# Optimization experiments

Hardware: AMD Instinct MI355X
Metric: run time of the kernel (lower is better)

Reference implementation:

```python
import jax, jax.numpy as jnp
import numpy as np

N_TOKENS = 4096   # flattened batch*seq tokens
D_MODEL = 1024
N_EXPERT = 8
D_HIDDEN = 1024   # expert FFN hidden size
TOP_K = 2


def setup_inputs() -> dict:
    key = jax.random.key(0)
    ks = jax.random.split(key, 4)
    f32 = jnp.float32
    return {
        "inp": jax.random.normal(ks[0], (N_TOKENS, D_MODEL), f32),
        "gate_w": jax.random.normal(ks[1], (D_MODEL, N_EXPERT), f32) * 0.02,
        "gate_b": jnp.zeros((N_EXPERT,), f32),
        "w1": jax.random.normal(ks[2], (N_EXPERT, D_MODEL, D_HIDDEN), f32) * 0.02,
        "b1": jnp.zeros((N_EXPERT, D_HIDDEN), f32),
        "w2": jax.random.normal(ks[3], (N_EXPERT, D_HIDDEN, D_MODEL), f32) * 0.02,
        "b2": jnp.zeros((N_EXPERT, D_MODEL), f32),
    }


def reference(inp, gate_w, gate_b, w1, b1, w2, b2):
    """FMoE forward: NaiveGate top-k -> dispatch -> per-expert FFN -> weighted combine.

    Math is identical to dispatch/grouped-GEMM/gather: since both top-k slots of a
    token see the same input, out[n] = sum_e coeff[n,e] * expert_e(inp[n]) where
    coeff[n,e] = sum_k softmax(top_vals)[n,k] * 1[top_idx[n,k] == e].
    """
    n_expert = gate_w.shape[-1]
    # NaiveGate: linear gate, top-k, softmax over the k selected logits
    logits = inp @ gate_w + gate_b                      # [N, E]
    top_val, top_idx = jax.lax.top_k(logits, TOP_K)     # [N, K]
    score = jax.nn.softmax(top_val, axis=-1)            # [N, K]
    # combine weights per (token, expert); top-k indices are distinct per token
    coeff = jnp.sum(
        jax.nn.one_hot(top_idx, n_expert, dtype=inp.dtype) * score[..., None],
        axis=1,
    )                                                   # [N, E]
    # expert FFN (exact-erf GeLU, matching torch.nn.functional.gelu)
    h = jax.nn.gelu(jnp.einsum('nd,edh->neh', inp, w1) + b1, approximate=False)  # [N, E, H]
    out = jnp.einsum('neh,ehd->nd', h * coeff[:, :, None], w2) + coeff @ b2      # [N, D]
    return out


if __name__ == "__main__":
    out = reference(**setup_inputs())
    print(out.shape, out.dtype)
```

## Files before the change

kernel.cpp:

```cpp
#include <hip/hip_runtime.h>
#include <math.h>

#define N_TOKENS 4096
#define D_MODEL  1024
#define N_EXPERT 8
#define D_HIDDEN 1024
#define N_POS    8192

typedef __bf16 bf16x8 __attribute__((ext_vector_type(8)));
typedef float  f32x4  __attribute__((ext_vector_type(4)));
typedef unsigned short u16x8 __attribute__((ext_vector_type(8)));

#define GLOBAL_AS __attribute__((address_space(1)))
#define LDS_AS    __attribute__((address_space(3)))

static __device__ __forceinline__ void async_ld16(const void* g, void* l) {
    __builtin_amdgcn_global_load_lds((GLOBAL_AS void*)g, (LDS_AS void*)l, 16, 0, 0);
}

static __device__ __forceinline__ unsigned short f2bf(float f) {
    unsigned int u = __builtin_bit_cast(unsigned int, f);
    u += 0x7fffu + ((u >> 16) & 1u);
    return (unsigned short)(u >> 16);
}
static __device__ __forceinline__ unsigned int pack2(float a, float b) {
    return (unsigned int)f2bf(a) | ((unsigned int)f2bf(b) << 16);
}
static __device__ __forceinline__ float bflo(unsigned int u) {
    return __builtin_bit_cast(float, u << 16);
}
static __device__ __forceinline__ float bfhi(unsigned int u) {
    return __builtin_bit_cast(float, u & 0xffff0000u);
}

__global__ __launch_bounds__(256) void convert_transpose_kernel(
    const float* __restrict__ w1, const float* __restrict__ w2,
    unsigned short* __restrict__ w1b, unsigned short* __restrict__ w2b)
{
    int mat = blockIdx.z;
    const float* src = (mat < 8) ? (w1 + (size_t)mat * 1048576)
                                 : (w2 + (size_t)(mat - 8) * 1048576);
    unsigned short* dst = (mat < 8) ? (w1b + (size_t)mat * 1048576)
                                    : (w2b + (size_t)(mat - 8) * 1048576);
    __shared__ float tile[64][68];
    int r0 = blockIdx.x * 64, c0 = blockIdx.y * 64;
    int tid = threadIdx.x;
    #pragma unroll
    for (int i = 0; i < 4; ++i) {
        int r = (tid >> 4) + i * 16;
        float4 v = *(const float4*)(src + (size_t)(r0 + r) * 1024 + c0 + (tid & 15) * 4);
        *(float4*)&tile[r][(tid & 15) * 4] = v;
    }
    __syncthreads();
    int dr = tid >> 2;
    #pragma unroll
    for (int p = 0; p < 2; ++p) {
        int ch = (tid & 3) + p * 4;
        u16x8 o;
        #pragma unroll
        for (int j = 0; j < 8; ++j) o[j] = f2bf(tile[ch * 8 + j][dr]);
        *(u16x8*)(dst + (size_t)(c0 + dr) * 1024 + r0 + ch * 8) = o;
    }
}

__global__ __launch_bounds__(256) void gate_kernel(
    const float* __restrict__ inp, const float* __restrict__ gate_w,
    const float* __restrict__ gate_b, int* __restrict__ cnts,
    int* __restrict__ emeta, float* __restrict__ stok)
{
    __shared__ int bcnt[8], base[8];
    __shared__ int tinfo[16];
    int tid = threadIdx.x, lane = tid & 63, wave = tid >> 6;
    if (tid < 8) bcnt[tid] = 0;
    __syncthreads();

    for (int t = 0; t < 4; ++t) {
        int ti = wave * 4 + t;
        int n  = blockIdx.x * 16 + ti;
        const float* ip = inp + (size_t)n * D_MODEL;
        float acc[8] = {0.f,0.f,0.f,0.f,0.f,0.f,0.f,0.f};
        for (int d0 = lane * 4; d0 < D_MODEL; d0 += 256) {
            float4 x = *(const float4*)(ip + d0);
            #pragma unroll
            for (int j = 0; j < 4; ++j) {
                float xv = (j == 0) ? x.x : (j == 1) ? x.y : (j == 2) ? x.z : x.w;
                float4 g0 = *(const float4*)(gate_w + (d0 + j) * 8);
                float4 g1 = *(const float4*)(gate_w + (d0 + j) * 8 + 4);
                acc[0] += xv * g0.x; acc[1] += xv * g0.y;
                acc[2] += xv * g0.z; acc[3] += xv * g0.w;
                acc[4] += xv * g1.x; acc[5] += xv * g1.y;
                acc[6] += xv * g1.z; acc[7] += xv * g1.w;
            }
        }
        #pragma unroll
        for (int off = 32; off > 0; off >>= 1)
            #pragma unroll
            for (int e = 0; e < 8; ++e)
                acc[e] += __shfl_xor(acc[e], off, 64);
        #pragma unroll
        for (int e = 0; e < 8; ++e) acc[e] += gate_b[e];

        int e0 = 0; float v0 = acc[0];
        #pragma unroll
        for (int e = 1; e < 8; ++e) if (acc[e] > v0) { v0 = acc[e]; e0 = e; }
        int e1 = -1; float v1 = -1e30f;
        #pragma unroll
        for (int e = 0; e < 8; ++e) if (e != e0 && acc[e] > v1) { v1 = acc[e]; e1 = e; }
        float tv = expf(v1 - v0);
        float s0 = 1.0f / (1.0f + tv);
        float s1 = tv / (1.0f + tv);

        if (lane == 0) {
            int r0 = atomicAdd(&bcnt[e0], 1);
            int r1 = atomicAdd(&bcnt[e1], 1);
            tinfo[ti] = e0 | (e1 << 4) | (r0 << 8) | (r1 << 20);
            stok[2 * n]     = s0;
            stok[2 * n + 1] = s1;
        }
    }
    __syncthreads();
    if (tid < 8) base[tid] = atomicAdd(&cnts[tid], bcnt[tid]);
    __syncthreads();
    if (tid < 16) {
        int n = blockIdx.x * 16 + tid;
        unsigned int inf = (unsigned int)tinfo[tid];
        int e0 = inf & 15, e1 = (inf >> 4) & 15;
        int p0 = base[e0] + ((inf >> 8) & 4095);
        int p1 = base[e1] + (int)(inf >> 20);
        emeta[n] = e0 | (e1 << 4) | (p0 << 8) | (p1 << 20);
    }
}

__global__ __launch_bounds__(256) void gather_kernel(
    const float* __restrict__ inp, const int* __restrict__ cnts,
    const int* __restrict__ emeta, unsigned short* __restrict__ Ag,
    int* __restrict__ tok2pos)
{
    int lane = threadIdx.x & 63, wave = threadIdx.x >> 6;
    int n = blockIdx.x * 4 + wave;
    unsigned int em = (unsigned int)emeta[n];
    int e0 = em & 15, e1 = (em >> 4) & 15;
    int p0 = (em >> 8) & 4095, p1 = (int)(em >> 20);
    int off0 = 0, off1 = 0;
    #pragma unroll
    for (int e = 0; e < 8; ++e) {
        int c = cnts[e];
        off0 += (e < e0) ? c : 0;
        off1 += (e < e1) ? c : 0;
    }
    int pos0 = off0 + p0, pos1 = off1 + p1;
    if (lane == 0) {
        tok2pos[2 * n]     = pos0;
        tok2pos[2 * n + 1] = pos1;
    }
    const float* ip = inp + (size_t)n * D_MODEL;
    unsigned short* r0 = Ag + (size_t)pos0 * D_MODEL;
    unsigned short* r1 = Ag + (size_t)pos1 * D_MODEL;
    for (int d = lane * 4; d < D_MODEL; d += 256) {
        float4 v = *(const float4*)(ip + d);
        uint2 u; u.x = pack2(v.x, v.y); u.y = pack2(v.z, v.w);
        *(uint2*)(r0 + d) = u;
        *(uint2*)(r1 + d) = u;
    }
}

__global__ __launch_bounds__(256, 4) void ffn1_kernel(
    const unsigned short* __restrict__ Ag, const unsigned short* __restrict__ w1b,
    const float* __restrict__ b1, const int* __restrict__ cnts,
    unsigned short* __restrict__ Hg)
{
    int bid = blockIdx.x;
    int e = bid & 7, nt = (bid >> 3) & 15, mt = bid >> 7;
    int off = 0, Ne = 0;
    #pragma unroll
    for (int i = 0; i < 8; ++i) {
        int c = cnts[i];
        off += (i < e) ? c : 0;
        Ne = (i == e) ? c : Ne;
    }
    int m0 = mt * 128;
    if (m0 >= Ne) return;
    int n0 = nt * 64;

    __shared__ unsigned short As[2 * 128 * 32];
    __shared__ unsigned short Bs[2 * 64 * 32];

    int tid = threadIdx.x, lane = tid & 63, wave = tid >> 6;
    int lrow = lane >> 2, lchunk = lane & 3;
    int csw8 = (lchunk ^ ((lrow >> 1) & 3)) * 8;

    int ga0 = off + m0 + wave * 32 + lrow;
    int ga1 = ga0 + 16;
    if (ga0 >= N_POS) ga0 = N_POS - 1;
    if (ga1 >= N_POS) ga1 = N_POS - 1;
    const unsigned short* aS0 = Ag + (size_t)ga0 * D_MODEL + csw8;
    const unsigned short* aS1 = Ag + (size_t)ga1 * D_MODEL + csw8;
    const unsigned short* bS = w1b + (size_t)e * D_MODEL * D_HIDDEN
                             + (size_t)(n0 + wave * 16 + lrow) * D_MODEL + csw8;
    unsigned short* aD0 = &As[(wave * 32) * 32];
    unsigned short* aD1 = &As[(wave * 32 + 16) * 32];
    unsigned short* bD  = &Bs[(wave * 16) * 32];

    f32x4 acc[4][2] = {};
    int wm = (wave & 1) * 64, wn = ((wave >> 1) & 1) * 32;
    int lane15 = lane & 15, quad = lane >> 4;
    int fro = (quad ^ ((lane15 >> 1) & 3)) * 8;

    for (int k0 = 0; k0 < D_MODEL; k0 += 64) {
        #pragma unroll
        for (int h = 0; h < 2; ++h) {
            int ko = k0 + h * 32;
            async_ld16(aS0 + ko, aD0 + h * 4096);
            async_ld16(aS1 + ko, aD1 + h * 4096);
            async_ld16(bS  + ko, bD  + h * 2048);
        }
        __syncthreads();
        #pragma unroll
        for (int h = 0; h < 2; ++h) {
            bf16x8 af[4], bf[2];
            #pragma unroll
            for (int t = 0; t < 4; ++t)
                af[t] = *(const bf16x8*)&As[h * 4096 + (wm + t * 16 + lane15) * 32 + fro];
            #pragma unroll
            for (int t = 0; t < 2; ++t)
                bf[t] = *(const bf16x8*)&Bs[h * 2048 + (wn + t * 16 + lane15) * 32 + fro];
            #pragma unroll
            for (int i = 0; i < 4; ++i)
                #pragma unroll
                for (int j = 0; j < 2; ++j)
                    acc[i][j] = __builtin_amdgcn_mfma_f32_16x16x32_bf16(
                        af[i], bf[j], acc[i][j], 0, 0, 0);
        }
        __syncthreads();
    }

    const float* bexp = b1 + (size_t)e * D_HIDDEN;
    #pragma unroll
    for (int j = 0; j < 2; ++j) {
        int gcol = n0 + wn + j * 16 + lane15;
        float bv = bexp[gcol];
        #pragma unroll
        for (int i = 0; i < 4; ++i) {
            int rowb = wm + i * 16 + quad * 4;
            #pragma unroll
            for (int r = 0; r < 4; ++r) {
                int row = rowb + r;
                if (m0 + row < Ne) {
                    float x = acc[i][j][r] + bv;
                    float gv = 0.5f * x * (1.0f + erff(x * 0.70710678118654752f));
                    Hg[(size_t)(off + m0 + row) * D_HIDDEN + gcol] = f2bf(gv);
                }
            }
        }
    }
}

__global__ __launch_bounds__(256, 4) void ffn2_kernel(
    const unsigned short* __restrict__ Hg, const unsigned short* __restrict__ w2b,
    const int* __restrict__ cnts, unsigned short* __restrict__ Og)
{
    int bid = blockIdx.x;
    int e = bid & 7, nt = (bid >> 3) & 15, mt = bid >> 7;
    int off = 0, Ne = 0;
    #pragma unroll
    for (int i = 0; i < 8; ++i) {
        int c = cnts[i];
        off += (i < e) ? c : 0;
        Ne = (i == e) ? c : Ne;
    }
    int m0 = mt * 128;
    if (m0 >= Ne) return;
    int n0 = nt * 64;

    __shared__ unsigned short As[2 * 128 * 32];
    __shared__ unsigned short Bs[2 * 64 * 32];

    int tid = threadIdx.x, lane = tid & 63, wave = tid >> 6;
    int lrow = lane >> 2, lchunk = lane & 3;
    int csw8 = (lchunk ^ ((lrow >> 1) & 3)) * 8;

    int ga0 = off + m0 + wave * 32 + lrow;
    int ga1 = ga0 + 16;
    if (ga0 >= N_POS) ga0 = N_POS - 1;
    if (ga1 >= N_POS) ga1 = N_POS - 1;
    const unsigned short* aS0 = Hg + (size_t)ga0 * D_HIDDEN + csw8;
    const unsigned short* aS1 = Hg + (size_t)ga1 * D_HIDDEN + csw8;
    const unsigned short* bS = w2b + (size_t)e * D_HIDDEN * D_MODEL
                             + (size_t)(n0 + wave * 16 + lrow) * D_HIDDEN + csw8;
    unsigned short* aD0 = &As[(wave * 32) * 32];
    unsigned short* aD1 = &As[(wave * 32 + 16) * 32];
    unsigned short* bD  = &Bs[(wave * 16) * 32];

    f32x4 acc[4][2] = {};
    int wm = (wave & 1) * 64, wn = ((wave >> 1) & 1) * 32;
    int lane15 = lane & 15, quad = lane >> 4;
    int fro = (quad ^ ((lane15 >> 1) & 3)) * 8;

    for (int k0 = 0; k0 < D_HIDDEN; k0 += 64) {
        #pragma unroll
        for (int h = 0; h < 2; ++h) {
            int ko = k0 + h * 32;
            async_ld16(aS0 + ko, aD0 + h * 4096);
            async_ld16(aS1 + ko, aD1 + h * 4096);
            async_ld16(bS  + ko, bD  + h * 2048);
        }
        __syncthreads();
        #pragma unroll
        for (int h = 0; h < 2; ++h) {
            bf16x8 af[4], bf[2];
            #pragma unroll
            for (int t = 0; t < 4; ++t)
                af[t] = *(const bf16x8*)&As[h * 4096 + (wm + t * 16 + lane15) * 32 + fro];
            #pragma unroll
            for (int t = 0; t < 2; ++t)
                bf[t] = *(const bf16x8*)&Bs[h * 2048 + (wn + t * 16 + lane15) * 32 + fro];
            #pragma unroll
            for (int i = 0; i < 4; ++i)
                #pragma unroll
                for (int j = 0; j < 2; ++j)
                    acc[i][j] = __builtin_amdgcn_mfma_f32_16x16x32_bf16(
                        af[i], bf[j], acc[i][j], 0, 0, 0);
        }
        __syncthreads();
    }

    #pragma unroll
    for (int j = 0; j < 2; ++j) {
        int gcol = n0 + wn + j * 16 + lane15;
        #pragma unroll
        for (int i = 0; i < 4; ++i) {
            int rowb = wm + i * 16 + quad * 4;
            #pragma unroll
            for (int r = 0; r < 4; ++r) {
                int row = rowb + r;
                if (m0 + row < Ne) {
                    Og[(size_t)(off + m0 + row) * D_MODEL + gcol] =
                        f2bf(acc[i][j][r]);
                }
            }
        }
    }
}

__global__ __launch_bounds__(256) void combine_kernel(
    const unsigned short* __restrict__ Og, const int* __restrict__ tok2pos,
    const float* __restrict__ stok, const int* __restrict__ emeta,
    const float* __restrict__ b2, float* __restrict__ out)
{
    int lane = threadIdx.x & 63, wave = threadIdx.x >> 6;
    int n = blockIdx.x * 4 + wave;
    int pos0 = tok2pos[2 * n], pos1 = tok2pos[2 * n + 1];
    float s0 = stok[2 * n], s1 = stok[2 * n + 1];
    unsigned int em = (unsigned int)emeta[n];
    int e0 = em & 15, e1 = (em >> 4) & 15;
    const unsigned short* o0 = Og + (size_t)pos0 * D_MODEL;
    const unsigned short* o1 = Og + (size_t)pos1 * D_MODEL;
    const float* bA = b2 + (size_t)e0 * D_MODEL;
    const float* bB = b2 + (size_t)e1 * D_MODEL;
    float* op = out + (size_t)n * D_MODEL;
    for (int d = lane * 4; d < D_MODEL; d += 256) {
        uint2 u0 = *(const uint2*)(o0 + d);
        uint2 u1 = *(const uint2*)(o1 + d);
        float4 xa = *(const float4*)(bA + d);
        float4 xb = *(const float4*)(bB + d);
        float4 r;
        r.x = s0 * (bflo(u0.x) + xa.x) + s1 * (bflo(u1.x) + xb.x);
        r.y = s0 * (bfhi(u0.x) + xa.y) + s1 * (bfhi(u1.x) + xb.y);
        r.z = s0 * (bflo(u0.y) + xa.z) + s1 * (bflo(u1.y) + xb.z);
        r.w = s0 * (bfhi(u0.y) + xa.w) + s1 * (bfhi(u1.y) + xb.w);
        *(float4*)(op + d) = r;
    }
}

extern "C" void kernel_launch(void* const* d_in, const int* in_sizes, int n_in,
                              void* d_out, int out_size, void* d_ws, size_t ws_size,
                              hipStream_t stream) {
    const float* inp    = (const float*)d_in[0];
    const float* gate_w = (const float*)d_in[1];
    const float* gate_b = (const float*)d_in[2];
    const float* w1     = (const float*)d_in[3];
    const float* b1     = (const float*)d_in[4];
    const float* w2     = (const float*)d_in[5];
    const float* b2     = (const float*)d_in[6];
    float* out = (float*)d_out;

    char* ws = (char*)d_ws;
    int*   cnts    = (int*)  (ws);
    int*   emeta   = (int*)  (ws + 4096);
    float* stok    = (float*)(ws + 65536);
    int*   tok2pos = (int*)  (ws + 131072);
    unsigned short* w2b = (unsigned short*)(ws + 1048576);
    unsigned short* Hg  = (unsigned short*)(ws + 17825792);
    unsigned short* w1b = (unsigned short*)(ws + 34603008);
    unsigned short* Og  = (unsigned short*)(ws + 34603008);

    unsigned short* Ag = (unsigned short*)d_out;

    hipMemsetAsync(cnts, 0, N_EXPERT * sizeof(int), stream);
    convert_transpose_kernel<<<dim3(16, 16, 16), 256, 0, stream>>>(w1, w2, w1b, w2b);
    gate_kernel<<<dim3(N_TOKENS / 16), 256, 0, stream>>>(
        inp, gate_w, gate_b, cnts, emeta, stok);
    gather_kernel<<<dim3(N_TOKENS / 4), 256, 0, stream>>>(
        inp, cnts, emeta, Ag, tok2pos);
    ffn1_kernel<<<dim3(4096), 256, 0, stream>>>(Ag, w1b, b1, cnts, Hg);
    ffn2_kernel<<<dim3(4096), 256, 0, stream>>>(Hg, w2b, cnts, Og);
    combine_kernel<<<dim3(N_TOKENS / 4), 256, 0, stream>>>(
        Og, tok2pos, stok, emeta, b2, out);
}
```

Before: 224.9 us.

## Replace gather copy with indexed A-loads in ffn1 via pos2tok map

Instead of materializing a permuted bf16 copy of the input per expert slot, the input is converted to bf16 once in the weight-conversion kernel. A small plan kernel then writes a position-to-token map, and ffn1 loads A rows indirectly through that map. The cnts memset is folded into the conversion kernel, the trailing __syncthreads in both GEMM loops is skipped on the last iteration, and combine recomputes positions from counts instead of reading tok2pos. This removes one launch and the gather's duplicated 16MB bf16 write, at the cost of scattered row loads in ffn1.

```diff
diff --git a/kernel.cpp b/kernel.cpp
--- a/kernel.cpp
+++ b/kernel.cpp
@@ -33,18 +33,36 @@
     return __builtin_bit_cast(float, u & 0xffff0000u);
 }
 
-__global__ __launch_bounds__(256) void convert_transpose_kernel(
+__global__ __launch_bounds__(256) void convert_kernel(
     const float* __restrict__ w1, const float* __restrict__ w2,
-    unsigned short* __restrict__ w1b, unsigned short* __restrict__ w2b)
-{
+    const float* __restrict__ inp,
+    unsigned short* __restrict__ w1b, unsigned short* __restrict__ w2b,
+    unsigned short* __restrict__ inp_bf, int* __restrict__ cnts)
+{
+    int tid = threadIdx.x;
+    if (blockIdx.x == 0 && blockIdx.y == 0 && blockIdx.z == 0 && tid < 8)
+        cnts[tid] = 0;
     int mat = blockIdx.z;
+    int r0 = blockIdx.x * 64, c0 = blockIdx.y * 64;
+
+    if (mat >= 16) {
+        const float* src = inp + (size_t)(mat - 16) * 1048576;
+        unsigned short* dst = inp_bf + (size_t)(mat - 16) * 1048576;
+        #pragma unroll
+        for (int i = 0; i < 4; ++i) {
+            int r = (tid >> 4) + i * 16;
+            float4 v = *(const float4*)(src + (size_t)(r0 + r) * 1024 + c0 + (tid & 15) * 4);
+            uint2 u; u.x = pack2(v.x, v.y); u.y = pack2(v.z, v.w);
+            *(uint2*)(dst + (size_t)(r0 + r) * 1024 + c0 + (tid & 15) * 4) = u;
+        }
+        return;
+    }
+
     const float* src = (mat < 8) ? (w1 + (size_t)mat * 1048576)
                                  : (w2 + (size_t)(mat - 8) * 1048576);
     unsigned short* dst = (mat < 8) ? (w1b + (size_t)mat * 1048576)
                                     : (w2b + (size_t)(mat - 8) * 1048576);
     __shared__ float tile[64][68];
-    int r0 = blockIdx.x * 64, c0 = blockIdx.y * 64;
-    int tid = threadIdx.x;
     #pragma unroll
     for (int i = 0; i < 4; ++i) {
         int r = (tid >> 4) + i * 16;
@@ -131,13 +149,11 @@
     }
 }
 
-__global__ __launch_bounds__(256) void gather_kernel(
-    const float* __restrict__ inp, const int* __restrict__ cnts,
-    const int* __restrict__ emeta, unsigned short* __restrict__ Ag,
-    int* __restrict__ tok2pos)
-{
-    int lane = threadIdx.x & 63, wave = threadIdx.x >> 6;
-    int n = blockIdx.x * 4 + wave;
+__global__ __launch_bounds__(256) void plan_kernel(
+    const int* __restrict__ cnts, const int* __restrict__ emeta,
+    int* __restrict__ pos2tok)
+{
+    int n = blockIdx.x * 256 + threadIdx.x;
     unsigned int em = (unsigned int)emeta[n];
     int e0 = em & 15, e1 = (em >> 4) & 15;
     int p0 = (em >> 8) & 4095, p1 = (int)(em >> 20);
@@ -148,26 +164,14 @@
         off0 += (e < e0) ? c : 0;
         off1 += (e < e1) ? c : 0;
     }
-    int pos0 = off0 + p0, pos1 = off1 + p1;
-    if (lane == 0) {
-        tok2pos[2 * n]     = pos0;
-        tok2pos[2 * n + 1] = pos1;
-    }
-    const float* ip = inp + (size_t)n * D_MODEL;
-    unsigned short* r0 = Ag + (size_t)pos0 * D_MODEL;
-    unsigned short* r1 = Ag + (size_t)pos1 * D_MODEL;
-    for (int d = lane * 4; d < D_MODEL; d += 256) {
-        float4 v = *(const float4*)(ip + d);
-        uint2 u; u.x = pack2(v.x, v.y); u.y = pack2(v.z, v.w);
-        *(uint2*)(r0 + d) = u;
-        *(uint2*)(r1 + d) = u;
-    }
+    pos2tok[off0 + p0] = n;
+    pos2tok[off1 + p1] = n;
 }
 
 __global__ __launch_bounds__(256, 4) void ffn1_kernel(
-    const unsigned short* __restrict__ Ag, const unsigned short* __restrict__ w1b,
+    const unsigned short* __restrict__ inp_bf, const unsigned short* __restrict__ w1b,
     const float* __restrict__ b1, const int* __restrict__ cnts,
-    unsigned short* __restrict__ Hg)
+    const int* __restrict__ pos2tok, unsigned short* __restrict__ Hg)
 {
     int bid = blockIdx.x;
     int e = bid & 7, nt = (bid >> 3) & 15, mt = bid >> 7;
@@ -184,17 +188,23 @@
 
     __shared__ unsigned short As[2 * 128 * 32];
     __shared__ unsigned short Bs[2 * 64 * 32];
+    __shared__ int rowtok[128];
 
     int tid = threadIdx.x, lane = tid & 63, wave = tid >> 6;
     int lrow = lane >> 2, lchunk = lane & 3;
     int csw8 = (lchunk ^ ((lrow >> 1) & 3)) * 8;
 
-    int ga0 = off + m0 + wave * 32 + lrow;
-    int ga1 = ga0 + 16;
-    if (ga0 >= N_POS) ga0 = N_POS - 1;
-    if (ga1 >= N_POS) ga1 = N_POS - 1;
-    const unsigned short* aS0 = Ag + (size_t)ga0 * D_MODEL + csw8;
-    const unsigned short* aS1 = Ag + (size_t)ga1 * D_MODEL + csw8;
+    if (tid < 128) {
+        int r = m0 + tid;
+        if (r >= Ne) r = Ne - 1;
+        rowtok[tid] = pos2tok[off + r];
+    }
+    __syncthreads();
+
+    const unsigned short* aS0 =
+        inp_bf + (size_t)rowtok[wave * 32 + lrow] * D_MODEL + csw8;
+    const unsigned short* aS1 =
+        inp_bf + (size_t)rowtok[wave * 32 + 16 + lrow] * D_MODEL + csw8;
     const unsigned short* bS = w1b + (size_t)e * D_MODEL * D_HIDDEN
                              + (size_t)(n0 + wave * 16 + lrow) * D_MODEL + csw8;
     unsigned short* aD0 = &As[(wave * 32) * 32];
@@ -231,7 +241,7 @@
                     acc[i][j] = __builtin_amdgcn_mfma_f32_16x16x32_bf16(
                         af[i], bf[j], acc[i][j], 0, 0, 0);
         }
-        __syncthreads();
+        if (k0 + 64 < D_MODEL) __syncthreads();
     }
 
     const float* bexp = b1 + (size_t)e * D_HIDDEN;
@@ -321,7 +331,7 @@
                     acc[i][j] = __builtin_amdgcn_mfma_f32_16x16x32_bf16(
                         af[i], bf[j], acc[i][j], 0, 0, 0);
         }
-        __syncthreads();
+        if (k0 + 64 < D_HIDDEN) __syncthreads();
     }
 
     #pragma unroll
@@ -343,16 +353,24 @@
 }
 
 __global__ __launch_bounds__(256) void combine_kernel(
-    const unsigned short* __restrict__ Og, const int* __restrict__ tok2pos,
-    const float* __restrict__ stok, const int* __restrict__ emeta,
+    const unsigned short* __restrict__ Og, const int* __restrict__ cnts,
+    const int* __restrict__ emeta, const float* __restrict__ stok,
     const float* __restrict__ b2, float* __restrict__ out)
 {
     int lane = threadIdx.x & 63, wave = threadIdx.x >> 6;
     int n = blockIdx.x * 4 + wave;
-    int pos0 = tok2pos[2 * n], pos1 = tok2pos[2 * n + 1];
-    float s0 = stok[2 * n], s1 = stok[2 * n + 1];
     unsigned int em = (unsigned int)emeta[n];
     int e0 = em & 15, e1 = (em >> 4) & 15;
+    int p0 = (em >> 8) & 4095, p1 = (int)(em >> 20);
+    int off0 = 0, off1 = 0;
+    #pragma unroll
+    for (int e = 0; e < 8; ++e) {
+        int c = cnts[e];
+        off0 += (e < e0) ? c : 0;
+        off1 += (e < e1) ? c : 0;
+    }
+    int pos0 = off0 + p0, pos1 = off1 + p1;
+    float s0 = stok[2 * n], s1 = stok[2 * n + 1];
     const unsigned short* o0 = Og + (size_t)pos0 * D_MODEL;
     const unsigned short* o1 = Og + (size_t)pos1 * D_MODEL;
     const float* bA = b2 + (size_t)e0 * D_MODEL;
@@ -388,22 +406,22 @@
     int*   cnts    = (int*)  (ws);
     int*   emeta   = (int*)  (ws + 4096);
     float* stok    = (float*)(ws + 65536);
-    int*   tok2pos = (int*)  (ws + 131072);
+    int*   pos2tok = (int*)  (ws + 131072);
     unsigned short* w2b = (unsigned short*)(ws + 1048576);
     unsigned short* Hg  = (unsigned short*)(ws + 17825792);
     unsigned short* w1b = (unsigned short*)(ws + 34603008);
     unsigned short* Og  = (unsigned short*)(ws + 34603008);
 
-    unsigned short* Ag = (unsigned short*)d_out;
-
-    hipMemsetAsync(cnts, 0, N_EXPERT * sizeof(int), stream);
-    convert_transpose_kernel<<<dim3(16, 16, 16), 256, 0, stream>>>(w1, w2, w1b, w2b);
+    unsigned short* inp_bf = (unsigned short*)d_out;
+
+    convert_kernel<<<dim3(16, 16, 20), 256, 0, stream>>>(
+        w1, w2, inp, w1b, w2b, inp_bf, cnts);
     gate_kernel<<<dim3(N_TOKENS / 16), 256, 0, stream>>>(
         inp, gate_w, gate_b, cnts, emeta, stok);
-    gather_kernel<<<dim3(N_TOKENS / 4), 256, 0, stream>>>(
-        inp, cnts, emeta, Ag, tok2pos);
-    ffn1_kernel<<<dim3(4096), 256, 0, stream>>>(Ag, w1b, b1, cnts, Hg);
+    plan_kernel<<<dim3(N_TOKENS / 256), 256, 0, stream>>>(cnts, emeta, pos2tok);
+    ffn1_kernel<<<dim3(4096), 256, 0, stream>>>(
+        inp_bf, w1b, b1, cnts, pos2tok, Hg);
     ffn2_kernel<<<dim3(4096), 256, 0, stream>>>(Hg, w2b, cnts, Og);
     combine_kernel<<<dim3(N_TOKENS / 4), 256, 0, stream>>>(
-        Og, tok2pos, stok, emeta, b2, out);
-}
+        Og, cnts, emeta, stok, b2, out);
+}
```

Result: no change. 224.5 us (-0.2%).
